# Kernel optimization log

Hardware: AMD Instinct MI355X
Metric: run time of the kernel (lower is better)

## Reference

```python
import jax, jax.numpy as jnp
import numpy as np

B, T, C = 2, 1024, 256
DH = 8          # deformable head num
HD = 64         # head_dim
HN = C // HD    # head_num = 4


def grid_sample_bilinear(img, grid):
    """torch.nn.functional.grid_sample (bilinear, align_corners=True) for a
    single-channel image. img: (B,H,W); grid: (B,Ho,Wo,2) with grid[...,0]=x
    (width coord), grid[...,1]=y (height coord), both in [-1,1]."""
    B_, H, W = img.shape
    gx = (grid[..., 0] + 1.0) * 0.5 * (W - 1)
    gy = (grid[..., 1] + 1.0) * 0.5 * (H - 1)
    x0 = jnp.floor(gx)
    y0 = jnp.floor(gy)
    wx = gx - x0
    wy = gy - y0
    flat_img = img.reshape(B_, -1)

    def gather(iy, ix):
        iy = jnp.clip(iy.astype(jnp.int32), 0, H - 1)
        ix = jnp.clip(ix.astype(jnp.int32), 0, W - 1)
        flat = (iy * W + ix).reshape(B_, -1)
        return jnp.take_along_axis(flat_img, flat, axis=1).reshape(iy.shape)

    out = (gather(y0, x0) * (1 - wy) * (1 - wx)
           + gather(y0, x0 + 1) * (1 - wy) * wx
           + gather(y0 + 1, x0) * wy * (1 - wx)
           + gather(y0 + 1, x0 + 1) * wy * wx)
    return out  # (B, Ho, Wo)


def setup_inputs() -> dict:
    key = jax.random.key(0)
    ks = jax.random.split(key, 8)
    s = 1.0 / np.sqrt(C)
    return {
        "x": jax.random.normal(ks[0], (B, T, C), jnp.float32),
        "W_off1": jax.random.normal(ks[1], (C, C), jnp.float32) * s,
        "b_off1": jnp.zeros((C,), jnp.float32),
        "W_off2": jax.random.normal(ks[2], (C, DH * C * 2), jnp.float32) * s,
        "b_off2": jnp.zeros((DH * C * 2,), jnp.float32),
        "Wq": jax.random.normal(ks[3], (C, C), jnp.float32) * s,
        "bq": jnp.zeros((C,), jnp.float32),
        "Wk": jax.random.normal(ks[4], (C, C), jnp.float32) * s,
        "bk": jnp.zeros((C,), jnp.float32),
        "Wv": jax.random.normal(ks[5], (C, C), jnp.float32) * s,
        "bv": jnp.zeros((C,), jnp.float32),
        "Wo": jax.random.normal(ks[6], (DH * C, C), jnp.float32) / np.sqrt(DH * C),
        "bo": jnp.zeros((C,), jnp.float32),
    }


def reference(x, W_off1, b_off1, W_off2, b_off2, Wq, bq, Wk, bk, Wv, bv, Wo, bo):
    B_, T_, C_ = x.shape
    # offset network: per-token MLP -> DH heads of (C,2) grid coords in [-1,1]
    h = jax.nn.gelu(x @ W_off1 + b_off1)
    off = jnp.tanh((h @ W_off2 + b_off2).reshape(B_, T_, DH, C_, 2))
    off = off.transpose(0, 2, 1, 3, 4).reshape(B_, DH * T_, C_, 2)
    # deformable token resampling: x tiled DH times along token axis acts as
    # a 1-channel image of size (DH*T, C); grid_sample(bilinear, align_corners)
    img = jnp.tile(x, (1, DH, 1))                       # B x (DH*T) x C
    xs = grid_sample_bilinear(img, off)                 # B x (DH*T) x C
    xs = xs.reshape(B_ * DH, T_, C_)
    # multi-head attention over resampled tokens
    q = (xs @ Wq + bq).reshape(B_ * DH, T_, HN, HD)
    k = (xs @ Wk + bk).reshape(B_ * DH, T_, HN, HD)
    v = (xs @ Wv + bv).reshape(B_ * DH, T_, HN, HD)
    scores = jnp.einsum('bnhd,bkhd->bhnk', q, k) / np.float32(np.sqrt(HD))
    A = jax.nn.softmax(scores, axis=-1)
    out = jnp.einsum('bhnk,bkhd->bnhd', A, v).reshape(B_ * DH, T_, HN * HD)
    # gather deformable heads back and project
    out = out.reshape(B_, DH, T_, HN * HD).transpose(0, 2, 1, 3).reshape(B_, T_, DH * HN * HD)
    return out @ Wo + bo
```

## Files before the change

kernel.cpp:

```cpp
#include <hip/hip_runtime.h>
#include <hip/hip_bf16.h>

typedef __attribute__((ext_vector_type(8))) _Float16 half8;
typedef __attribute__((ext_vector_type(4))) float f32x4;
typedef __attribute__((ext_vector_type(16))) float f32x16;
typedef __attribute__((ext_vector_type(2))) unsigned uint2v;
typedef __attribute__((ext_vector_type(4))) unsigned uint4v;
typedef __attribute__((ext_vector_type(2), aligned(4))) float f32x2a;

#define MFMAH(a, b, c) __builtin_amdgcn_mfma_f32_16x16x32_f16((a), (b), (c), 0, 0, 0)
#define MFMA32(a, b, c) __builtin_amdgcn_mfma_f32_32x32x16_f16((a), (b), (c), 0, 0, 0)

__device__ __forceinline__ short f2h(float v) { _Float16 h = (_Float16)v; return __builtin_bit_cast(short, h); }
__device__ __forceinline__ f32x4 fzero() { f32x4 z = {0.f, 0.f, 0.f, 0.f}; return z; }
__device__ __forceinline__ float u2f(unsigned u) { return __builtin_bit_cast(float, u); }
__device__ __forceinline__ unsigned f2u(float f) { return __builtin_bit_cast(unsigned, f); }

__device__ __forceinline__ void gl16(const void* g, void* l) {
    __builtin_amdgcn_global_load_lds((const __attribute__((address_space(1))) unsigned*)g,
                                     (__attribute__((address_space(3))) unsigned*)l, 16, 0, 0);
}

__device__ __forceinline__ float fast_tanh(float z) {
    float E = __expf(2.f * z);
    return 1.f - 2.f / (E + 1.f);
}

__device__ __forceinline__ float gelu_tanh(float v) {
    float u = 0.7978845608028654f * (v + 0.044715f * v * v * v);
    return 0.5f * v * (1.f + fast_tanh(u));
}


__global__ __launch_bounds__(256) void split_w2_k(const float* __restrict__ w, short* __restrict__ dst) {
    __shared__ float t[64][65];
    const int tid = threadIdx.x;
    const int bk = blockIdx.x >> 6, bn = blockIdx.x & 63;
    const int k0 = bk * 64, n0 = bn * 64;
#pragma unroll
    for (int p = 0; p < 16; ++p) {
        int idx = p * 256 + tid, r = idx >> 6, c = idx & 63;
        t[r][c] = w[(long)(k0 + r) * 4096 + n0 + c];
    }
    __syncthreads();
#pragma unroll
    for (int p = 0; p < 16; ++p) {
        int idx = p * 256 + tid, nr = idx >> 6, kc = idx & 63;
        float v = t[kc][nr];
        _Float16 w1 = (_Float16)v;
        _Float16 w2 = (_Float16)(v - (float)w1);
        long base = (long)(n0 + nr) * 768 + k0 + kc;
        dst[base]       = __builtin_bit_cast(short, w1);
        dst[base + 256] = __builtin_bit_cast(short, w1);
        dst[base + 512] = __builtin_bit_cast(short, w2);
    }
}

__global__ void qkv_prep_k(const float* __restrict__ Wq, const float* __restrict__ Wk,
                           const float* __restrict__ Wv, short* __restrict__ dst) {
    int i = blockIdx.x * 256 + threadIdx.x;
    int n = i >> 8, k = i & 255;
    const float* s = (n < 256) ? Wq : (n < 512) ? Wk : Wv;
    dst[i] = f2h(s[k * 256 + (n & 255)]);
}

__global__ void wo_prep_k(const float* __restrict__ Wo, short* __restrict__ dst) {
    int i = blockIdx.x * 256 + threadIdx.x;
    int n = i >> 11, k = i & 2047;
    dst[i] = f2h(Wo[k * 256 + n]);
}


__global__ __launch_bounds__(256) void gemm1_k(const float* __restrict__ x, const float* __restrict__ W,
                                               const float* __restrict__ bias, short* __restrict__ hs) {
    __shared__ float As[64][17];
    __shared__ float Bs[16][68];
    const int tid = threadIdx.x;
    const int bm = blockIdx.x >> 2, bn = blockIdx.x & 3;
    const int m0 = bm * 64, n0 = bn * 64;
    const int ty = tid >> 4, tx = tid & 15;
    float acc[4][4] = {};
    const int ar = tid >> 2, ak = (tid & 3) << 2;
    const int bk = tid >> 4, bc = (tid & 15) << 2;

    for (int k0 = 0; k0 < 256; k0 += 16) {
        __syncthreads();
        float4 av = *(const float4*)(x + (m0 + ar) * 256 + k0 + ak);
        As[ar][ak + 0] = av.x; As[ar][ak + 1] = av.y; As[ar][ak + 2] = av.z; As[ar][ak + 3] = av.w;
        *(float4*)&Bs[bk][bc] = *(const float4*)(W + (k0 + bk) * 256 + n0 + bc);
        __syncthreads();
#pragma unroll
        for (int kk = 0; kk < 16; ++kk) {
            float a_[4], b_[4];
#pragma unroll
            for (int i = 0; i < 4; ++i) a_[i] = As[ty * 4 + i][kk];
            *(float4*)b_ = *(const float4*)&Bs[kk][tx * 4];
#pragma unroll
            for (int i = 0; i < 4; ++i)
#pragma unroll
                for (int j = 0; j < 4; ++j) acc[i][j] += a_[i] * b_[j];
        }
    }
#pragma unroll
    for (int i = 0; i < 4; ++i) {
        int row = m0 + ty * 4 + i;
#pragma unroll
        for (int j = 0; j < 4; ++j) {
            int col = n0 + tx * 4 + j;
            float v = gelu_tanh(acc[i][j] + bias[col]);
            _Float16 h1 = (_Float16)v;
            _Float16 h2 = (_Float16)(v - (float)h1);
            hs[row * 768 + col]       = __builtin_bit_cast(short, h1);
            hs[row * 768 + 256 + col] = __builtin_bit_cast(short, h2);
            hs[row * 768 + 512 + col] = __builtin_bit_cast(short, h1);
        }
    }
}


template <int EPI>
__global__ __launch_bounds__(256, 2) void gemm128(
    const short* __restrict__ A, const short* __restrict__ BT,
    const float* __restrict__ b0, const float* __restrict__ b1, const float* __restrict__ b2,
    void* __restrict__ out0, void* __restrict__ out1, void* __restrict__ out2,
    int M, int N, int K, int lda, int ldb, const float* __restrict__ xsrc)
{
    __shared__ short lds[16384];
    short* As0 = lds;
    short* As1 = lds + 4096;
    short* Bs0 = lds + 8192;
    short* Bs1 = lds + 12288;

    const int tid = threadIdx.x;
    const int lane = tid & 63, w = tid >> 6;
    const int rl = lane & 15, g = lane >> 4;
    const int wr = w >> 1, wc = w & 1;
    const int bid = blockIdx.x;
    int bm, bn;
    if (EPI == 1) {
        bm = bid >> 5;
        bn = (bid & 7) * 4 + ((bid >> 3) & 3);
    } else if (EPI == 2) {
        int s = bid >> 3;
        bm = (bid & 7) * 16 + s / 6;
        bn = s - (s / 6) * 6;
    } else {
        const int nb = N >> 7;
        bm = bid / nb;
        bn = bid % nb;
    }
    const int m0 = bm << 7, n0 = bn << 7;

    if (EPI == 3) { A += blockIdx.y << 8; BT += blockIdx.y << 8; }

    f32x4 acc[4][4];
#pragma unroll
    for (int m = 0; m < 4; ++m)
#pragma unroll
        for (int n = 0; n < 4; ++n) acc[m][n] = fzero();

    const short* ap = A + (long)(m0 + w * 32 + (lane >> 2)) * lda + ((lane & 3) << 3);
    const short* bp = BT + (long)(n0 + w * 32 + (lane >> 2)) * ldb + ((lane & 3) << 3);
    const int woff = w * 1024;

#define STAGE(dA, dB, kk) do { \
        gl16(ap + (kk), (dA) + woff); \
        gl16(ap + (kk) + 16 * lda, (dA) + woff + 512); \
        gl16(bp + (kk), (dB) + woff); \
        gl16(bp + (kk) + 16 * ldb, (dB) + woff + 512); } while (0)

    const int nt_ = K >> 5;
    STAGE(As0, Bs0, 0);
    for (int t = 0; t < nt_; ++t) {
        const short* cA = (t & 1) ? As1 : As0;
        const short* cB = (t & 1) ? Bs1 : Bs0;
        short* nA = (t & 1) ? As0 : As1;
        short* nB = (t & 1) ? Bs0 : Bs1;
        if (t + 1 < nt_) {
            STAGE(nA, nB, (t + 1) << 5);
            asm volatile("s_waitcnt vmcnt(4)" ::: "memory");
        } else {
            asm volatile("s_waitcnt vmcnt(0)" ::: "memory");
        }
        __builtin_amdgcn_s_barrier();
        half8 af[4], bf[4];
#pragma unroll
        for (int m = 0; m < 4; ++m) af[m] = *(const half8*)&cA[(wr * 64 + m * 16 + rl) * 32 + g * 8];
#pragma unroll
        for (int n = 0; n < 4; ++n) bf[n] = *(const half8*)&cB[(wc * 64 + n * 16 + rl) * 32 + g * 8];
#pragma unroll
        for (int m = 0; m < 4; ++m)
#pragma unroll
            for (int n = 0; n < 4; ++n) acc[m][n] = MFMAH(af[m], bf[n], acc[m][n]);
        __builtin_amdgcn_s_barrier();
    }
#undef STAGE

    if (EPI == 1) {
        const int d = n0 >> 9, c0 = (n0 >> 1) & 255;
#pragma unroll
        for (int m = 0; m < 4; ++m)
#pragma unroll
            for (int nt = 0; nt < 4; ++nt) {
                const int col = n0 + wc * 64 + nt * 16 + rl;
                float o4[4], po4[4];
                const float bb = b0[col];
#pragma unroll
                for (int j = 0; j < 4; ++j) o4[j] = fast_tanh(acc[m][nt][j] + bb);
#pragma unroll
                for (int j = 0; j < 4; ++j) po4[j] = __shfl_xor(o4[j], 1);
                const int jlo = (rl & 1) ? 2 : 0;
                const int cl = (wc * 64 + nt * 16 + rl) >> 1;
#pragma unroll
                for (int u = 0; u < 2; ++u) {
                    const int j = jlo + u;
                    float gx = (rl & 1) ? po4[j] : o4[j];
                    float gy = (rl & 1) ? o4[j] : po4[j];
                    gx = (gx + 1.f) * 127.5f;
                    gy = (gy + 1.f) * 4095.5f;
                    float x0f = floorf(gx), y0f = floorf(gy);
                    float wx = gx - x0f, wy = gy - y0f;
                    int ix0 = (int)x0f, iy0 = (int)y0f;
                    int iy1 = min(iy0 + 1, 8191);
                    iy0 = max(min(iy0, 8191), 0);
                    iy1 = max(iy1, 0);
                    int ixc = max(min(ix0, 254), 0);
                    const int rowl = wr * 64 + m * 16 + g * 4 + j;
                    const int b = (m0 + rowl) >> 10;
                    const float* xb = xsrc + b * 262144;
                    int r0 = (iy0 & 1023) << 8, r1 = (iy1 & 1023) << 8;
                    f32x2a fx0 = *(const f32x2a*)(xb + r0 + ixc);
                    f32x2a fx1 = *(const f32x2a*)(xb + r1 + ixc);
                    float v00 = (ix0 >= 255) ? fx0[1] : fx0[0];
                    float v01 = (ix0 < 0)    ? fx0[0] : fx0[1];
                    float v10 = (ix0 >= 255) ? fx1[1] : fx1[0];
                    float v11 = (ix0 < 0)    ? fx1[0] : fx1[1];
                    float r = v00 * (1.f - wy) * (1.f - wx) + v01 * (1.f - wy) * wx
                            + v10 * wy * (1.f - wx) + v11 * wy * wx;
                    lds[rowl * 72 + cl] = f2h(r);
                }
            }
        __syncthreads();
        const int b = m0 >> 10, t0 = m0 & 1023;
        short* xo = (short*)out0 + ((long)(b * 8 + d) * 1024 + t0) * 256 + c0;
#pragma unroll
        for (int p = 0; p < 4; ++p) {
            int idx = p * 256 + tid, rowl = idx >> 3, ch = idx & 7;
            *(half8*)(xo + rowl * 256 + ch * 8) = *(const half8*)&lds[rowl * 72 + ch * 8];
        }
    } else if (EPI == 2) {
#pragma unroll
        for (int m = 0; m < 4; ++m)
#pragma unroll
            for (int nt = 0; nt < 4; ++nt) {
                const int cl = wc * 64 + nt * 16 + rl;
                const int col = n0 + cl;
#pragma unroll
                for (int j = 0; j < 4; ++j) {
                    const int tl = wr * 64 + m * 16 + g * 4 + j;
                    float v;
                    int slot;
                    if (bn < 2) {
                        v = (acc[m][nt][j] + b0[col]) * 0.18033688011112042f;
                        slot = tl * 128 + cl;
                    } else if (bn < 4) {
                        v = acc[m][nt][j] + b1[(bn - 2) * 128 + cl];
                        int hl = cl >> 6, dd = cl & 63;
                        int c = dd >> 4, hi2 = (dd >> 3) & 1, e = dd & 7;
                        int kkl = tl >> 5, l31t = tl & 31;
                        slot = (hl * 4 + kkl) * 2048 + (c * 64 + hi2 * 32 + l31t) * 8 + e;
                    } else {
                        v = acc[m][nt][j] + b2[(bn - 4) * 128 + cl];
                        int hl = cl >> 6, d = cl & 63;
                        int kkl = tl >> 5, chi = (tl >> 4) & 1, hi2 = (tl >> 3) & 1, e = tl & 7;
                        int c = chi * 2 + (d >> 5);
                        slot = (hl * 4 + kkl) * 2048 + (c * 64 + hi2 * 32 + (d & 31)) * 8 + e;
                    }
                    lds[slot] = f2h(v);
                }
            }
        __syncthreads();
        const int bh = m0 >> 10;
        if (bn < 2) {
            short* qo = (short*)out0 + (long)m0 * 256 + n0;
#pragma unroll
            for (int p = 0; p < 8; ++p) {
                int idx = p * 256 + tid, rowl = idx >> 4, ch = idx & 15;
                *(half8*)(qo + rowl * 256 + ch * 8) = *(const half8*)&lds[rowl * 128 + ch * 8];
            }
        } else {
            short* dst = (bn < 4) ? (short*)out1 : (short*)out2;
            const int hb = (bn < 4) ? (bn - 2) * 2 : (bn - 4) * 2;
            const int kk0 = (m0 & 1023) >> 5;
#pragma unroll
            for (int p = 0; p < 8; ++p) {
                int idx = p * 256 + tid, til = idx >> 8, wit = idx & 255;
                int hl = til >> 2, kkl = til & 3;
                long base = (((long)(bh * 4 + hb + hl) * 32) + kk0 + kkl) * 2048;
                *(half8*)(dst + base + wit * 8) = *(const half8*)&lds[til * 2048 + wit * 8];
            }
        }
    } else {
        float* op = (float*)out0 + (long)blockIdx.y * M * N;
#pragma unroll
        for (int m = 0; m < 4; ++m)
#pragma unroll
            for (int nt = 0; nt < 4; ++nt) {
                const int col = n0 + wc * 64 + nt * 16 + rl;
#pragma unroll
                for (int j = 0; j < 4; ++j) {
                    const long grow = m0 + wr * 64 + m * 16 + g * 4 + j;
                    op[grow * N + col] = acc[m][nt][j];
                }
            }
    }
}

__global__ void reduce_out_k(const float* __restrict__ p, const float* __restrict__ bo,
                             float* __restrict__ out) {
    int i = blockIdx.x * 256 + threadIdx.x;
    float s = bo[i & 255];
#pragma unroll
    for (int ks = 0; ks < 8; ++ks) s += p[ks * 524288 + i];
    out[i] = s;
}


__global__ __launch_bounds__(256) void attn_k(const short* __restrict__ q, const short* __restrict__ kc,
                                              const short* __restrict__ vc, short* __restrict__ oc) {
    __shared__ short kv[8192];
    const int tid = threadIdx.x;
    const int lane = tid & 63, w = tid >> 6;
    const int l31 = lane & 31, hi = lane >> 5;
    const int bhh = blockIdx.x & 63;
    const int bh = bhh >> 2, h = bhh & 3;
    const int q0 = (blockIdx.x >> 6) * 128 + w * 32;

    const short* qb = q + (long)bh * 262144 + h * 64;
    const short* kt = kc + (long)bhh * 65536;
    const short* vt = vc + (long)bhh * 65536;

    half8 qf[4];
#pragma unroll
    for (int c = 0; c < 4; ++c)
        qf[c] = *(const half8*)(qb + (long)(q0 + l31) * 256 + c * 16 + hi * 8);

    float m_ = -1e30f, l_ = 0.f;
    f32x16 O0, O1;
#pragma unroll
    for (int r = 0; r < 16; ++r) { O0[r] = 0.f; O1[r] = 0.f; }

    const int sw = w * 512 + lane * 8;

#define KVSTAGE(kk, b) do { \
        gl16(kt + (kk) * 2048 + sw, &kv[(b) * 4096 + w * 512]); \
        gl16(vt + (kk) * 2048 + sw, &kv[(b) * 4096 + 2048 + w * 512]); } while (0)

    KVSTAGE(0, 0);
    __syncthreads();
    for (int kk = 0; kk < 32; ++kk) {
        const int b = kk & 1;
        if (kk + 1 < 32) KVSTAGE(kk + 1, b ^ 1);
        half8 KD[4], VD[4];
#pragma unroll
        for (int c = 0; c < 4; ++c) {
            KD[c] = *(const half8*)&kv[b * 4096 + c * 512 + lane * 8];
            VD[c] = *(const half8*)&kv[b * 4096 + 2048 + c * 512 + lane * 8];
        }
        f32x16 S;
#pragma unroll
        for (int r = 0; r < 16; ++r) S[r] = 0.f;
#pragma unroll
        for (int c = 0; c < 4; ++c) S = MFMA32(KD[c], qf[c], S);
        float t8[8];
#pragma unroll
        for (int r = 0; r < 8; ++r) t8[r] = fmaxf(S[2 * r], S[2 * r + 1]);
        float mx = fmaxf(fmaxf(fmaxf(t8[0], t8[1]), fmaxf(t8[2], t8[3])),
                         fmaxf(fmaxf(t8[4], t8[5]), fmaxf(t8[6], t8[7])));
        uint2v sp = __builtin_amdgcn_permlane32_swap(f2u(mx), f2u(mx), false, false);
        mx = fmaxf(u2f(sp[0]), u2f(sp[1]));
        if (__any(mx > m_ + 8.f)) {
            float mn = fmaxf(m_, mx);
            float sc = exp2f(m_ - mn);
            m_ = mn;
            l_ *= sc;
#pragma unroll
            for (int r = 0; r < 16; ++r) { O0[r] *= sc; O1[r] *= sc; }
        }
        float p[16];
#pragma unroll
        for (int r = 0; r < 16; ++r) p[r] = exp2f(S[r] - m_);
        float s8[8];
#pragma unroll
        for (int r = 0; r < 8; ++r) s8[r] = p[2 * r] + p[2 * r + 1];
        float rs = (((s8[0] + s8[1]) + (s8[2] + s8[3])) + ((s8[4] + s8[5]) + (s8[6] + s8[7])));
        uint2v sq = __builtin_amdgcn_permlane32_swap(f2u(rs), f2u(rs), false, false);
        rs = u2f(sq[0]) + u2f(sq[1]);
        l_ += rs;
        half8 PA[2];
#pragma unroll
        for (int c = 0; c < 2; ++c) {
            const int o = c * 8;
            unsigned a0 = f2u(__builtin_bit_cast(float, __builtin_amdgcn_cvt_pkrtz(p[o + 0], p[o + 1])));
            unsigned b0v = f2u(__builtin_bit_cast(float, __builtin_amdgcn_cvt_pkrtz(p[o + 4], p[o + 5])));
            unsigned a1 = f2u(__builtin_bit_cast(float, __builtin_amdgcn_cvt_pkrtz(p[o + 2], p[o + 3])));
            unsigned b1v = f2u(__builtin_bit_cast(float, __builtin_amdgcn_cvt_pkrtz(p[o + 6], p[o + 7])));
            uint2v r0 = __builtin_amdgcn_permlane32_swap(a0, b0v, false, false);
            uint2v r1 = __builtin_amdgcn_permlane32_swap(a1, b1v, false, false);
            uint4v wpk = {r0[0], r1[0], r0[1], r1[1]};
            PA[c] = __builtin_bit_cast(half8, wpk);
        }
        O0 = MFMA32(VD[0], PA[0], O0);
        O1 = MFMA32(VD[1], PA[0], O1);
        O0 = MFMA32(VD[2], PA[1], O0);
        O1 = MFMA32(VD[3], PA[1], O1);
        __syncthreads();
    }
#undef KVSTAGE

    const float inv = 1.f / l_;
    const int b = bh >> 3, d = bh & 7;
    const int t = q0 + l31;
    short* ob = oc + ((long)(b * 1024 + t) * 8 + d) * 256 + h * 64;
#pragma unroll
    for (int rr = 0; rr < 8; ++rr) {
        int dvb = (rr & 1) * 2 + 8 * (rr >> 1) + 4 * hi;
        unsigned u0 = (unsigned short)f2h(O0[2 * rr] * inv) | ((unsigned)(unsigned short)f2h(O0[2 * rr + 1] * inv) << 16);
        unsigned u1 = (unsigned short)f2h(O1[2 * rr] * inv) | ((unsigned)(unsigned short)f2h(O1[2 * rr + 1] * inv) << 16);
        *(unsigned*)(ob + dvb) = u0;
        *(unsigned*)(ob + 32 + dvb) = u1;
    }
}


extern "C" void kernel_launch(void* const* d_in, const int* in_sizes, int n_in,
                              void* d_out, int out_size, void* d_ws, size_t ws_size,
                              hipStream_t stream) {
    const float* x     = (const float*)d_in[0];
    const float* Woff1 = (const float*)d_in[1];
    const float* boff1 = (const float*)d_in[2];
    const float* Woff2 = (const float*)d_in[3];
    const float* boff2 = (const float*)d_in[4];
    const float* Wq    = (const float*)d_in[5];
    const float* bq    = (const float*)d_in[6];
    const float* Wk    = (const float*)d_in[7];
    const float* bk    = (const float*)d_in[8];
    const float* Wv    = (const float*)d_in[9];
    const float* bv    = (const float*)d_in[10];
    const float* Wo    = (const float*)d_in[11];
    const float* bo    = (const float*)d_in[12];

    char* ws = (char*)d_ws;
    short* hsplit = (short*)(ws + 0);
    short* B2T    = (short*)(ws + 3145728);
    short* cat    = (short*)(ws + 0);
    short* Wtqkv  = (short*)(ws + 9437184);
    short* WtoT   = (short*)(ws + 9830400);
    short* xs     = (short*)(ws + 10878976);
    short* qbuf   = (short*)(ws + 19267584);
    short* kcoal  = (short*)(ws + 27656192);
    short* vcoal  = (short*)(ws + 36044800);
    float* parts  = (float*)(ws + 44433408);

    split_w2_k<<<256, 256, 0, stream>>>(Woff2, B2T);
    qkv_prep_k<<<768, 256, 0, stream>>>(Wq, Wk, Wv, Wtqkv);
    wo_prep_k<<<2048, 256, 0, stream>>>(Wo, WtoT);

    gemm1_k<<<128, 256, 0, stream>>>(x, Woff1, boff1, hsplit);

    gemm128<1><<<(2048 / 128) * (4096 / 128), 256, 0, stream>>>(
        hsplit, B2T, boff2, nullptr, nullptr, xs, nullptr, nullptr, 2048, 4096, 768, 768, 768, x);

    gemm128<2><<<(16384 / 128) * (768 / 128), 256, 0, stream>>>(
        xs, Wtqkv, bq, bk, bv, qbuf, kcoal, vcoal, 16384, 768, 256, 256, 256, nullptr);

    attn_k<<<512, 256, 0, stream>>>(qbuf, kcoal, vcoal, cat);

    gemm128<3><<<dim3((2048 / 128) * (256 / 128), 8), 256, 0, stream>>>(
        cat, WtoT, nullptr, nullptr, nullptr, parts, nullptr, nullptr, 2048, 256, 256, 2048, 2048, nullptr);
    reduce_out_k<<<2048, 256, 0, stream>>>(parts, bo, (float*)d_out);
}
```

Measured before the change: 155.9 us.

## Precompute bilinear quad table and fuse weight prep kernels

```diff
diff --git a/kernel.cpp b/kernel.cpp
--- a/kernel.cpp
+++ b/kernel.cpp
@@ -6,7 +6,6 @@
 typedef __attribute__((ext_vector_type(16))) float f32x16;
 typedef __attribute__((ext_vector_type(2))) unsigned uint2v;
 typedef __attribute__((ext_vector_type(4))) unsigned uint4v;
-typedef __attribute__((ext_vector_type(2), aligned(4))) float f32x2a;
 
 #define MFMAH(a, b, c) __builtin_amdgcn_mfma_f32_16x16x32_f16((a), (b), (c), 0, 0, 0)
 #define MFMA32(a, b, c) __builtin_amdgcn_mfma_f32_32x32x16_f16((a), (b), (c), 0, 0, 0)
@@ -32,42 +31,57 @@
 }
 
 
-__global__ __launch_bounds__(256) void split_w2_k(const float* __restrict__ w, short* __restrict__ dst) {
+__global__ __launch_bounds__(256) void prep_all_k(
+    const float* __restrict__ x, const float* __restrict__ Woff2,
+    const float* __restrict__ Wq, const float* __restrict__ Wk, const float* __restrict__ Wv,
+    const float* __restrict__ Wo,
+    short* __restrict__ B2T, short* __restrict__ Wtqkv, short* __restrict__ WtoT,
+    f32x4* __restrict__ Q)
+{
     __shared__ float t[64][65];
     const int tid = threadIdx.x;
-    const int bk = blockIdx.x >> 6, bn = blockIdx.x & 63;
-    const int k0 = bk * 64, n0 = bn * 64;
-#pragma unroll
-    for (int p = 0; p < 16; ++p) {
-        int idx = p * 256 + tid, r = idx >> 6, c = idx & 63;
-        t[r][c] = w[(long)(k0 + r) * 4096 + n0 + c];
-    }
-    __syncthreads();
-#pragma unroll
-    for (int p = 0; p < 16; ++p) {
-        int idx = p * 256 + tid, nr = idx >> 6, kc = idx & 63;
-        float v = t[kc][nr];
-        _Float16 w1 = (_Float16)v;
-        _Float16 w2 = (_Float16)(v - (float)w1);
-        long base = (long)(n0 + nr) * 768 + k0 + kc;
-        dst[base]       = __builtin_bit_cast(short, w1);
-        dst[base + 256] = __builtin_bit_cast(short, w1);
-        dst[base + 512] = __builtin_bit_cast(short, w2);
-    }
-}
-
-__global__ void qkv_prep_k(const float* __restrict__ Wq, const float* __restrict__ Wk,
-                           const float* __restrict__ Wv, short* __restrict__ dst) {
-    int i = blockIdx.x * 256 + threadIdx.x;
-    int n = i >> 8, k = i & 255;
-    const float* s = (n < 256) ? Wq : (n < 512) ? Wk : Wv;
-    dst[i] = f2h(s[k * 256 + (n & 255)]);
-}
-
-__global__ void wo_prep_k(const float* __restrict__ Wo, short* __restrict__ dst) {
-    int i = blockIdx.x * 256 + threadIdx.x;
-    int n = i >> 11, k = i & 2047;
-    dst[i] = f2h(Wo[k * 256 + n]);
+    const int bid = blockIdx.x;
+    if (bid < 256) {
+        const int bk = bid >> 6, bn = bid & 63;
+        const int k0 = bk * 64, n0 = bn * 64;
+#pragma unroll
+        for (int p = 0; p < 16; ++p) {
+            int idx = p * 256 + tid, r = idx >> 6, c = idx & 63;
+            t[r][c] = Woff2[(long)(k0 + r) * 4096 + n0 + c];
+        }
+        __syncthreads();
+#pragma unroll
+        for (int p = 0; p < 16; ++p) {
+            int idx = p * 256 + tid, nr = idx >> 6, kc = idx & 63;
+            float v = t[kc][nr];
+            _Float16 w1 = (_Float16)v;
+            _Float16 w2 = (_Float16)(v - (float)w1);
+            long base = (long)(n0 + nr) * 768 + k0 + kc;
+            B2T[base]       = __builtin_bit_cast(short, w1);
+            B2T[base + 256] = __builtin_bit_cast(short, w1);
+            B2T[base + 512] = __builtin_bit_cast(short, w2);
+        }
+    } else if (bid < 1024) {
+        int i = (bid - 256) * 256 + tid;
+        int n = i >> 8, k = i & 255;
+        const float* s = (n < 256) ? Wq : (n < 512) ? Wk : Wv;
+        Wtqkv[i] = f2h(s[k * 256 + (n & 255)]);
+    } else if (bid < 3072) {
+        int i = (bid - 1024) * 256 + tid;
+        int n = i >> 11, k = i & 2047;
+        WtoT[i] = f2h(Wo[k * 256 + n]);
+    } else {
+        int i = (bid - 3072) * 256 + tid;
+        int b = i >> 18, r = (i >> 8) & 1023, c = i & 255;
+        const float* xb = x + (b << 18);
+        int r1 = (r + 1) & 1023, c1 = (c + 1) & 255;
+        f32x4 qv;
+        qv[0] = xb[(r << 8) + c];
+        qv[1] = xb[(r << 8) + c1];
+        qv[2] = xb[(r1 << 8) + c];
+        qv[3] = xb[(r1 << 8) + c1];
+        Q[i] = qv;
+    }
 }
 
 
@@ -119,11 +133,11 @@
 
 
 template <int EPI>
-__global__ __launch_bounds__(256, 2) void gemm128(
+__global__ __launch_bounds__(256, 3) void gemm128(
     const short* __restrict__ A, const short* __restrict__ BT,
     const float* __restrict__ b0, const float* __restrict__ b1, const float* __restrict__ b2,
     void* __restrict__ out0, void* __restrict__ out1, void* __restrict__ out2,
-    int M, int N, int K, int lda, int ldb, const float* __restrict__ xsrc)
+    int M, int N, int K, int lda, int ldb, const f32x4* __restrict__ Q)
 {
     __shared__ short lds[16384];
     short* As0 = lds;
@@ -221,22 +235,11 @@
                     float x0f = floorf(gx), y0f = floorf(gy);
                     float wx = gx - x0f, wy = gy - y0f;
                     int ix0 = (int)x0f, iy0 = (int)y0f;
-                    int iy1 = min(iy0 + 1, 8191);
-                    iy0 = max(min(iy0, 8191), 0);
-                    iy1 = max(iy1, 0);
-                    int ixc = max(min(ix0, 254), 0);
                     const int rowl = wr * 64 + m * 16 + g * 4 + j;
                     const int b = (m0 + rowl) >> 10;
-                    const float* xb = xsrc + b * 262144;
-                    int r0 = (iy0 & 1023) << 8, r1 = (iy1 & 1023) << 8;
-                    f32x2a fx0 = *(const f32x2a*)(xb + r0 + ixc);
-                    f32x2a fx1 = *(const f32x2a*)(xb + r1 + ixc);
-                    float v00 = (ix0 >= 255) ? fx0[1] : fx0[0];
-                    float v01 = (ix0 < 0)    ? fx0[0] : fx0[1];
-                    float v10 = (ix0 >= 255) ? fx1[1] : fx1[0];
-                    float v11 = (ix0 < 0)    ? fx1[0] : fx1[1];
-                    float r = v00 * (1.f - wy) * (1.f - wx) + v01 * (1.f - wy) * wx
-                            + v10 * wy * (1.f - wx) + v11 * wy * wx;
+                    f32x4 qv = Q[((long)b << 18) + ((iy0 & 1023) << 8) + ix0];
+                    float r = qv[0] * (1.f - wy) * (1.f - wx) + qv[1] * (1.f - wy) * wx
+                            + qv[2] * wy * (1.f - wx) + qv[3] * wy * wx;
                     lds[rowl * 72 + cl] = f2h(r);
                 }
             }
@@ -460,16 +463,15 @@
     short* qbuf   = (short*)(ws + 19267584);
     short* kcoal  = (short*)(ws + 27656192);
     short* vcoal  = (short*)(ws + 36044800);
+    f32x4* Qt     = (f32x4*)(ws + 44433408);
     float* parts  = (float*)(ws + 44433408);
 
-    split_w2_k<<<256, 256, 0, stream>>>(Woff2, B2T);
-    qkv_prep_k<<<768, 256, 0, stream>>>(Wq, Wk, Wv, Wtqkv);
-    wo_prep_k<<<2048, 256, 0, stream>>>(Wo, WtoT);
+    prep_all_k<<<5120, 256, 0, stream>>>(x, Woff2, Wq, Wk, Wv, Wo, B2T, Wtqkv, WtoT, Qt);
 
     gemm1_k<<<128, 256, 0, stream>>>(x, Woff1, boff1, hsplit);
 
-    gemm128<1><<<(2048 / 128) * (4096 / 128), 256, 0, stream>>>(
-        hsplit, B2T, boff2, nullptr, nullptr, xs, nullptr, nullptr, 2048, 4096, 768, 768, 768, x);
+    gemm128<1><<<512, 256, 0, stream>>>(
+        hsplit, B2T, boff2, nullptr, nullptr, xs, nullptr, nullptr, 2048, 4096, 768, 768, 768, Qt);
 
     gemm128<2><<<(16384 / 128) * (768 / 128), 256, 0, stream>>>(
         xs, Wtqkv, bq, bk, bv, qbuf, kcoal, vcoal, 16384, 768, 256, 256, 256, nullptr);
```

New measurement: 150.0 us. 1.04x faster.
